# Kernel optimization log

Hardware: AMD Instinct MI355X
Metric: run time of the kernel (lower is better)

Reference implementation:

```python
import jax, jax.numpy as jnp
import numpy as np

B, L = 512, 260          # batch, raw input length
N_EMB, E_DIM = 8192, 128 * 65
NC = 16                   # num_classes


def setup_inputs() -> dict:
    key = jax.random.key(0)
    ks = jax.random.split(key, 12)
    rn = lambda k, shp, s: jax.random.normal(k, shp, jnp.float32) * s
    return {
        "x": rn(ks[0], (B, L), 1.0),
        # VQ codebook, init uniform(-1/K, 1/K) as in reference VQ-VAE
        "codebook": jax.random.uniform(ks[1], (N_EMB, E_DIM), jnp.float32, -1.0 / N_EMB, 1.0 / N_EMB),
        # encoder: Conv1d(1,64,k4,s2,p1) -> ReLU -> Conv1d(64,128,k4,s2,p1)
        "conv1_w": rn(ks[2], (64, 1, 4), 0.3), "conv1_b": jnp.zeros((64,), jnp.float32),
        "conv2_w": rn(ks[3], (128, 64, 4), 0.06), "conv2_b": jnp.zeros((128,), jnp.float32),
        # decoder: ConvT1d(128,64,k4,s2,p1) -> ReLU -> ConvT1d(64,1,k4,s2,p1); torch weight layout (in,out,k)
        "dec1_w": rn(ks[4], (128, 64, 4), 0.04), "dec1_b": jnp.zeros((64,), jnp.float32),
        "dec2_w": rn(ks[5], (64, 1, 4), 0.06), "dec2_b": jnp.zeros((1,), jnp.float32),
        # multitask head: Linear(4160, NC); torch layout (out,in)
        "mt_w": rn(ks[6], (NC, 4160), 0.015), "mt_b": jnp.zeros((NC,), jnp.float32),
        # adversary head: Linear(4160,256)->ReLU->Linear(256,128)->ReLU->Linear(128,NC)
        "adv_w1": rn(ks[7], (256, 4160), 0.015), "adv_b1": jnp.zeros((256,), jnp.float32),
        "adv_w2": rn(ks[8], (128, 256), 0.06), "adv_b2": jnp.zeros((128,), jnp.float32),
        "adv_w3": rn(ks[9], (NC, 128), 0.09), "adv_b3": jnp.zeros((NC,), jnp.float32),
        "beta": 0.25,
    }


def _conv1d(x, w, b, stride):
    # x: [B,C,L], w: [O,I,K] (torch Conv1d layout), padding=1
    y = jax.lax.conv_general_dilated(x, w, (stride,), [(1, 1)],
                                     dimension_numbers=("NCH", "OIH", "NCH"))
    return y + b[None, :, None]


def _convT1d(x, w, b, stride, k=4, p=1):
    # torch ConvTranspose1d(in,out,k,stride=s,padding=p); w: [I,O,K]
    # == dilated conv with lhs_dilation=s, padding=k-1-p, spatially-flipped, IO-swapped kernel
    wt = jnp.flip(w, -1).transpose(1, 0, 2)  # [O,I,K]
    pad = k - 1 - p
    y = jax.lax.conv_general_dilated(x, wt, (1,), [(pad, pad)], lhs_dilation=(stride,),
                                     dimension_numbers=("NCH", "OIH", "NCH"))
    return y + b[None, :, None]


def _forward(x, codebook, conv1_w, conv1_b, conv2_w, conv2_b,
             dec1_w, dec1_b, dec2_w, dec2_b, mt_w, mt_b,
             adv_w1, adv_b1, adv_w2, adv_b2, adv_w3, adv_b3, beta):
    sg = jax.lax.stop_gradient
    xb = x[:, None, :]                                      # x.unsqueeze_(1) -> [B,1,260]
    h = jax.nn.relu(_conv1d(xb, conv1_w, conv1_b, 2))       # [B,64,130]
    z_e = _conv1d(h, conv2_w, conv2_b, 2)                   # [B,128,65]
    b = z_e.shape[0]

    # ---- VectorQuantizer: cdist^2 / argmin / gather / commitment loss ----
    z = z_e.reshape(b, -1)                                  # [B,8320]
    d = (jnp.sum(z * z, axis=1, keepdims=True)
         + jnp.sum(codebook * codebook, axis=1)[None, :]
         - 2.0 * (z @ codebook.T))                          # [B,N_EMB]
    idx = jnp.argmin(d, axis=1)                             # [B]
    zq_raw = codebook[idx].reshape(z_e.shape)               # gather -> [B,128,65]
    emb_loss = (jnp.mean((sg(zq_raw) - z_e) ** 2)
                + beta * jnp.mean((zq_raw - sg(z_e)) ** 2))
    z_q = z_e + sg(zq_raw - z_e)                            # straight-through
    counts = jnp.zeros((codebook.shape[0],), z.dtype).at[idx].add(1.0)
    e_mean = counts / b
    perplexity = jnp.exp(-jnp.sum(e_mean * jnp.log(e_mean + 1e-10)))

    # ---- heads operate on z_e halves ----
    mt = z_e[:, :64, :].reshape(b, -1) @ mt_w.T + mt_b      # [B,NC]
    a = jax.nn.relu(z_e[:, 64:, :].reshape(b, -1) @ adv_w1.T + adv_b1)
    a = jax.nn.relu(a @ adv_w2.T + adv_b2)
    adv = a @ adv_w3.T + adv_b3                             # [B,NC]

    # ---- decoder on quantized codes ----
    hd = jax.nn.relu(_convT1d(z_q, dec1_w, dec1_b, 2))      # [B,64,130]
    x_hat = _convT1d(hd, dec2_w, dec2_b, 2)                 # [B,1,260]
    return emb_loss, x_hat, mt, adv, perplexity


def reference(x, codebook, conv1_w, conv1_b, conv2_w, conv2_b,
              dec1_w, dec1_b, dec2_w, dec2_b, mt_w, mt_b,
              adv_w1, adv_b1, adv_w2, adv_b2, adv_w3, adv_b3, beta):
    return _forward(x, codebook, conv1_w, conv1_b, conv2_w, conv2_b,
                    dec1_w, dec1_b, dec2_w, dec2_b, mt_w, mt_b,
                    adv_w1, adv_b1, adv_w2, adv_b2, adv_w3, adv_b3, beta)
```

## Files before the change

kernel.cpp:

```cpp
#include <hip/hip_runtime.h>
#include <stdint.h>

typedef __attribute__((ext_vector_type(8))) short s8v;
typedef __attribute__((ext_vector_type(4))) float f4v;

#define OUT_XHAT 1
#define OUT_MT   133121
#define OUT_ADV  141313
#define OUT_PERP 149505

#define WS_COUNTS   0
#define WS_EMB      8192
#define WS_A1       8256
#define WS_CN       139328
#define WS_ZN2      147520
#define WS_ZL1      148032
#define WS_CBL1     148544
#define WS_ZERO_N   156736
#define WS_ZE       156736
#define WS_SC0      4416576
#define WS_SC1      8610880
#define WS_HD       8676416
#define WS_W2T      12936256
#define WS_WE       12969024
#define WS_WO       12985408
#define WS_W2TA     13001792
#define WS_IDX      13034560
#define WS_ZPK      13035136
#define WS_CBT      15165056

__device__ __forceinline__ short f2bf(float f) {
  uint32_t u = __float_as_uint(f);
  u = (u + 0x7FFFu + ((u >> 16) & 1u)) >> 16;
  return (short)u;
}

__device__ __forceinline__ void gl_lds16(const void* g, void* l) {
  __builtin_amdgcn_global_load_lds(
      (const __attribute__((address_space(1))) void*)g,
      (__attribute__((address_space(3))) void*)l, 16, 0, 0);
}

__global__ void k_initprep(float* __restrict__ W, const float* __restrict__ c2w,
                           const float* __restrict__ d1w,
                           const float* __restrict__ aw2) {
  int id = blockIdx.x * 256 + threadIdx.x;
  if (id < WS_ZERO_N) W[id] = 0.f;
  float* w2t = W + WS_W2T;
  float* We = W + WS_WE;
  float* Wo = W + WS_WO;
  float* w2ta = W + WS_W2TA;
  if (id < 32768) {
    int c = id & 127, ik = id >> 7;
    int i = ik >> 2, k = ik & 3;
    w2t[id] = c2w[(c * 64 + i) * 4 + k];
    int kk = id >> 7;
    w2ta[id] = aw2[(id & 127) * 256 + kk];
  }
  if (id < 16384) {
    int o = id & 63, is = id >> 6;
    int i = is >> 1, s = is & 1;
    We[id] = d1w[(i * 64 + o) * 4 + (3 - 2 * s)];
    Wo[id] = d1w[(i * 64 + o) * 4 + (2 - 2 * s)];
  }
}

__device__ __forceinline__ void packmat_body(
    const float* __restrict__ src, short* __restrict__ dst,
    float* __restrict__ nrm2, float* __restrict__ l1, int R, int nb, int bid,
    int tid, short* tile, float* rsq, float* rl1) {
  int n0 = (bid % nb) * 64;
  int k0 = (bid / nb) * 64;
  int nr = tid >> 2, qc = tid & 3;
  const float* sp = src + (size_t)(n0 + nr) * 8320 + k0 + qc * 16;
  float v[16];
  *(float4*)&v[0] = *(const float4*)(sp);
  *(float4*)&v[4] = *(const float4*)(sp + 4);
  *(float4*)&v[8] = *(const float4*)(sp + 8);
  *(float4*)&v[12] = *(const float4*)(sp + 12);
  float sq = 0.f, sl = 0.f;
#pragma unroll
  for (int i = 0; i < 16; ++i) {
    sq = fmaf(v[i], v[i], sq);
    sl += fabsf(v[i]);
  }
  union { short s[8]; int4 q; } u0, u1;
#pragma unroll
  for (int j = 0; j < 8; ++j) {
    u0.s[j] = f2bf(v[j]);
    u1.s[j] = f2bf(v[8 + j]);
  }
  *(int4*)&tile[((qc * 2 + 0) * 64 + nr) * 8] = u0.q;
  *(int4*)&tile[((qc * 2 + 1) * 64 + nr) * 8] = u1.q;
  rsq[tid] = sq;
  rl1[tid] = sl;
  __syncthreads();
  if (tid < 64) {
    float s = rsq[tid * 4] + rsq[tid * 4 + 1] + rsq[tid * 4 + 2] + rsq[tid * 4 + 3];
    float t = rl1[tid * 4] + rl1[tid * 4 + 1] + rl1[tid * 4 + 2] + rl1[tid * 4 + 3];
    atomicAdd(&nrm2[n0 + tid], s);
    atomicAdd(&l1[n0 + tid], t);
  }
  int kc = tid >> 5, nn = (tid & 31) * 2;
  size_t ob = ((size_t)(k0 / 8 + kc) * R + n0 + nn) * 8;
  *(int4*)&dst[ob] = *(int4*)&tile[(kc * 64 + nn) * 8];
  *(int4*)&dst[ob + 8] = *(int4*)&tile[(kc * 64 + nn + 1) * 8];
}

__global__ __launch_bounds__(256) void k_megaA(
    const float* __restrict__ x, const float* __restrict__ c1w,
    const float* __restrict__ c1b, const float* __restrict__ w2t,
    const float* __restrict__ c2b, float* __restrict__ zebuf,
    const float* __restrict__ cb, short* __restrict__ cbt,
    float* __restrict__ cn, float* __restrict__ cbl1) {
  __shared__ __align__(16) char smem[28032];
  int bid = blockIdx.x, tid = threadIdx.x;
  if (bid < 520) {
    float* At = (float*)smem;
    float* Bt = At + 2048;
    float* xs = Bt + 4096;
    float* w1s = xs + 520;
    float* b1s = w1s + 256;
    int row0 = bid * 64;
    int tm = (tid & 15) * 4;
    int tn = (tid >> 4) * 8;
    int sr = tid & 63;
    int sj0 = (tid >> 6) * 8;
    int rowm = row0 + sr;
    int gb = rowm / 65;
    int gt = rowm - gb * 65;
    int gb0 = row0 / 65;
    int xrow = gb - gb0;
    int tpos = 2 * gt - 1;
    int bkr = tid >> 3;
    int bnc = (tid & 7) * 16;
    for (int u = tid; u < 520; u += 256) {
      int rr = gb0 + (u >= 260 ? 1 : 0);
      if (rr > 511) rr = 511;
      xs[u] = x[rr * 260 + (u >= 260 ? u - 260 : u)];
    }
    if (tid < 256) w1s[tid] = c1w[tid];
    if (tid < 64) b1s[tid] = c1b[tid];
    __syncthreads();
    float acc[4][8];
#pragma unroll
    for (int i = 0; i < 4; ++i)
#pragma unroll
      for (int j = 0; j < 8; ++j) acc[i][j] = 0.f;
    for (int k0i = 0; k0i < 256; k0i += 32) {
      float av[8];
#pragma unroll
      for (int u = 0; u < 8; ++u) {
        int jj = k0i + sj0 + u;
        int cc = jj >> 2;
        int kk = jj & 3;
        int p = tpos + kk;
        float hv = 0.f;
        if (p >= 0 && p < 130) {
          float a = b1s[cc];
          int base = 2 * p - 1;
#pragma unroll
          for (int k = 0; k < 4; ++k) {
            int xp = base + k;
            float xv = (xp >= 0 && xp < 260) ? xs[xrow * 260 + xp] : 0.f;
            a = fmaf(xv, w1s[cc * 4 + k], a);
          }
          hv = fmaxf(a, 0.f);
        }
        av[u] = hv;
      }
      float bvv[16];
#pragma unroll
      for (int u = 0; u < 16; ++u) bvv[u] = w2t[(k0i + bkr) * 128 + bnc + u];
      __syncthreads();
#pragma unroll
      for (int u = 0; u < 8; ++u) At[(sj0 + u) * 64 + sr] = av[u];
#pragma unroll
      for (int u = 0; u < 16; ++u) Bt[bkr * 128 + bnc + u] = bvv[u];
      __syncthreads();
#pragma unroll
      for (int kk = 0; kk < 32; ++kk) {
        float a0 = At[kk * 64 + tm + 0];
        float a1 = At[kk * 64 + tm + 1];
        float a2 = At[kk * 64 + tm + 2];
        float a3 = At[kk * 64 + tm + 3];
#pragma unroll
        for (int j = 0; j < 8; ++j) {
          float bv = Bt[kk * 128 + tn + j];
          acc[0][j] = fmaf(a0, bv, acc[0][j]);
          acc[1][j] = fmaf(a1, bv, acc[1][j]);
          acc[2][j] = fmaf(a2, bv, acc[2][j]);
          acc[3][j] = fmaf(a3, bv, acc[3][j]);
        }
      }
    }
#pragma unroll
    for (int i = 0; i < 4; ++i) {
      int rr = row0 + tm + i;
      int b = rr / 65, t = rr - b * 65;
#pragma unroll
      for (int j = 0; j < 8; ++j) {
        int n = tn + j;
        zebuf[(size_t)b * 8320 + (size_t)n * 65 + t] = acc[i][j] + c2b[n];
      }
    }
  } else {
    short* tile = (short*)smem;
    float* rsq = (float*)(smem + 8192);
    float* rl1 = rsq + 256;
    packmat_body(cb, cbt, cn, cbl1, 8192, 128, bid - 520, tid, tile, rsq, rl1);
  }
}

__global__ __launch_bounds__(256) void k_megaB(
    const float* __restrict__ z_e, const float* __restrict__ mtw,
    const float* __restrict__ mtb, const float* __restrict__ aw1,
    short* __restrict__ zpk, float* __restrict__ zn2, float* __restrict__ zl1,
    float* __restrict__ a1, float* __restrict__ out) {
  __shared__ __align__(16) char smem[16384];
  int bid = blockIdx.x, tid = threadIdx.x;
  if (bid < 320) {
    float* At = (float*)smem;
    float* Bt = At + 2048;
    int ksp = bid % 10;
    int nt = (bid / 10) & 3;
    int mt = bid / 40;
    int m0 = mt * 64, n0 = nt * 64, kb = ksp * 416;
    int tm = (tid & 15) * 4, tn = (tid >> 4) * 4;
    int sr = tid & 63, sj = (tid >> 6) * 8;
    const float* za = z_e + (size_t)(m0 + sr) * 8320 + 4160 + kb + sj;
    const float* wb = aw1 + (size_t)(n0 + sr) * 4160 + kb + sj;
    float acc[4][4];
#pragma unroll
    for (int i = 0; i < 4; ++i)
#pragma unroll
      for (int j = 0; j < 4; ++j) acc[i][j] = 0.f;
    for (int k0 = 0; k0 < 416; k0 += 32) {
      float4 av0 = *(const float4*)(za + k0);
      float4 av1 = *(const float4*)(za + k0 + 4);
      float4 bv0 = *(const float4*)(wb + k0);
      float4 bv1 = *(const float4*)(wb + k0 + 4);
      __syncthreads();
      At[(sj + 0) * 64 + sr] = av0.x; At[(sj + 1) * 64 + sr] = av0.y;
      At[(sj + 2) * 64 + sr] = av0.z; At[(sj + 3) * 64 + sr] = av0.w;
      At[(sj + 4) * 64 + sr] = av1.x; At[(sj + 5) * 64 + sr] = av1.y;
      At[(sj + 6) * 64 + sr] = av1.z; At[(sj + 7) * 64 + sr] = av1.w;
      Bt[(sj + 0) * 64 + sr] = bv0.x; Bt[(sj + 1) * 64 + sr] = bv0.y;
      Bt[(sj + 2) * 64 + sr] = bv0.z; Bt[(sj + 3) * 64 + sr] = bv0.w;
      Bt[(sj + 4) * 64 + sr] = bv1.x; Bt[(sj + 5) * 64 + sr] = bv1.y;
      Bt[(sj + 6) * 64 + sr] = bv1.z; Bt[(sj + 7) * 64 + sr] = bv1.w;
      __syncthreads();
#pragma unroll
      for (int kk = 0; kk < 32; ++kk) {
        float4 aa = *(const float4*)&At[kk * 64 + tm];
        float4 bb = *(const float4*)&Bt[kk * 64 + tn];
        acc[0][0] = fmaf(aa.x, bb.x, acc[0][0]); acc[0][1] = fmaf(aa.x, bb.y, acc[0][1]);
        acc[0][2] = fmaf(aa.x, bb.z, acc[0][2]); acc[0][3] = fmaf(aa.x, bb.w, acc[0][3]);
        acc[1][0] = fmaf(aa.y, bb.x, acc[1][0]); acc[1][1] = fmaf(aa.y, bb.y, acc[1][1]);
        acc[1][2] = fmaf(aa.y, bb.z, acc[1][2]); acc[1][3] = fmaf(aa.y, bb.w, acc[1][3]);
        acc[2][0] = fmaf(aa.z, bb.x, acc[2][0]); acc[2][1] = fmaf(aa.z, bb.y, acc[2][1]);
        acc[2][2] = fmaf(aa.z, bb.z, acc[2][2]); acc[2][3] = fmaf(aa.z, bb.w, acc[2][3]);
        acc[3][0] = fmaf(aa.w, bb.x, acc[3][0]); acc[3][1] = fmaf(aa.w, bb.y, acc[3][1]);
        acc[3][2] = fmaf(aa.w, bb.z, acc[3][2]); acc[3][3] = fmaf(aa.w, bb.w, acc[3][3]);
      }
    }
#pragma unroll
    for (int i = 0; i < 4; ++i)
#pragma unroll
      for (int j = 0; j < 4; ++j)
        atomicAdd(&a1[(size_t)(m0 + tm + i) * 256 + n0 + tn + j], acc[i][j]);
  } else if (bid < 832) {
    float* red = (float*)smem;
    int b = bid - 320;
    int wave = tid >> 6, lane = tid & 63;
    const float* zr = z_e + (size_t)b * 8320;
    float acc[16];
#pragma unroll
    for (int n = 0; n < 16; ++n) acc[n] = 0.f;
    for (int k4 = tid; k4 < 1040; k4 += 256) {
      float4 zv = *(const float4*)&zr[k4 * 4];
#pragma unroll
      for (int n = 0; n < 16; ++n) {
        float4 wv = *(const float4*)&mtw[n * 4160 + k4 * 4];
        float a = acc[n];
        a = fmaf(zv.x, wv.x, a);
        a = fmaf(zv.y, wv.y, a);
        a = fmaf(zv.z, wv.z, a);
        a = fmaf(zv.w, wv.w, a);
        acc[n] = a;
      }
    }
#pragma unroll
    for (int n = 0; n < 16; ++n) {
      float v = acc[n];
      for (int off = 32; off > 0; off >>= 1) v += __shfl_down(v, off);
      if (lane == 0) red[n * 4 + wave] = v;
    }
    __syncthreads();
    if (tid < 16) {
      float s = red[tid * 4] + red[tid * 4 + 1] + red[tid * 4 + 2] + red[tid * 4 + 3];
      out[OUT_MT + b * 16 + tid] = s + mtb[tid];
    }
  } else {
    short* tile = (short*)smem;
    float* rsq = (float*)(smem + 8192);
    float* rl1 = rsq + 256;
    packmat_body(z_e, zpk, zn2, zl1, 512, 8, bid - 832, tid, tile, rsq, rl1);
  }
}

__global__ __launch_bounds__(256) void k_scores(const short* __restrict__ cbt,
                                                const short* __restrict__ zpk,
                                                const float* __restrict__ cn,
                                                float* __restrict__ sc0,
                                                float* __restrict__ sc1) {
  __shared__ short As[8 * 128 * 8];
  __shared__ short Bs[8 * 128 * 8];
  int bid = blockIdx.x;
  int kh = bid & 1, nt = (bid >> 1) & 63, mt = bid >> 7;
  int tid = threadIdx.x;
  int wave = tid >> 6, lane = tid & 63;
  int q = lane >> 4, r16 = lane & 15;
  int m0 = mt * 128, n0 = nt * 128;
  int cb8 = kh * 520;
  int rb = (wave >> 1) * 64, cw = (wave & 1) * 64;

  f4v acc[4][4];
#pragma unroll
  for (int i = 0; i < 4; ++i)
#pragma unroll
    for (int j = 0; j < 4; ++j)
#pragma unroll
      for (int r = 0; r < 4; ++r) acc[i][j][r] = 0.f;

  for (int ks = 0; ks < 65; ++ks) {
    int c0 = cb8 + ks * 8;
    __syncthreads();
#pragma unroll
    for (int i = 0; i < 4; ++i) {
      int kc = wave * 2 + (i & 1);
      int h = (i >> 1) * 64;
      size_t gk = (size_t)(c0 + kc);
      gl_lds16(zpk + (gk * 512 + m0 + h + lane) * 8, &As[(kc * 128 + h) * 8]);
      gl_lds16(cbt + (gk * 8192 + n0 + h + lane) * 8, &Bs[(kc * 128 + h) * 8]);
    }
    __syncthreads();
    s8v af[2][4], bfr[2][4];
#pragma unroll
    for (int g = 0; g < 2; ++g) {
      int kq = (g * 4 + q) * 128;
#pragma unroll
      for (int i = 0; i < 4; ++i) {
        af[g][i] = *(const s8v*)&As[(kq + rb + i * 16 + r16) * 8];
        bfr[g][i] = *(const s8v*)&Bs[(kq + cw + i * 16 + r16) * 8];
      }
    }
#pragma unroll
    for (int g = 0; g < 2; ++g)
#pragma unroll
      for (int mi = 0; mi < 4; ++mi)
#pragma unroll
        for (int ni = 0; ni < 4; ++ni)
          acc[mi][ni] = __builtin_amdgcn_mfma_f32_16x16x32_bf16(
              af[g][mi], bfr[g][ni], acc[mi][ni], 0, 0, 0);
  }

  float* sc = kh ? sc1 : sc0;
#pragma unroll
  for (int mi = 0; mi < 4; ++mi) {
#pragma unroll
    for (int ni = 0; ni < 4; ++ni) {
      int col = n0 + cw + ni * 16 + r16;
      float cnv = kh ? 0.f : cn[col];
#pragma unroll
      for (int r = 0; r < 4; ++r) {
        int row = m0 + rb + mi * 16 + q * 4 + r;
        sc[(size_t)row * 8192 + col] = -2.f * acc[mi][ni][r] + cnv;
      }
    }
  }
}

__global__ __launch_bounds__(256) void k_argming(
    const float* __restrict__ s0, const float* __restrict__ s1,
    const float* __restrict__ z_e, const float* __restrict__ cb,
    const float* __restrict__ zn2, const float* __restrict__ cn,
    int* __restrict__ idx, float* __restrict__ counts,
    float* __restrict__ emb_acc) {
  __shared__ float srow[8192];
  __shared__ float red[256];
  __shared__ int cand[128];
  __shared__ float cval[128];
  __shared__ int ccnt;
  __shared__ int bsel;
  int b = blockIdx.x, tid = threadIdx.x;
  const float* r0 = s0 + (size_t)b * 8192;
  const float* r1 = s1 + (size_t)b * 8192;
  float mn = 1e30f;
  for (int j4 = tid; j4 < 2048; j4 += 256) {
    float4 a = *(const float4*)&r0[j4 * 4];
    float4 c = *(const float4*)&r1[j4 * 4];
    float4 v;
    v.x = a.x + c.x; v.y = a.y + c.y; v.z = a.z + c.z; v.w = a.w + c.w;
    *(float4*)&srow[j4 * 4] = v;
    mn = fminf(mn, fminf(fminf(v.x, v.y), fminf(v.z, v.w)));
  }
  red[tid] = mn;
  __syncthreads();
  for (int st = 128; st > 0; st >>= 1) {
    if (tid < st) red[tid] = fminf(red[tid], red[tid + st]);
    __syncthreads();
  }
  float minv = red[0];
  float margin = sqrtf(zn2[b]) * (1.0f / 131072.0f) + 1e-4f;
  if (tid == 0) ccnt = 0;
  __syncthreads();
  float thr = minv + margin;
  for (int j = tid; j < 8192; j += 256) {
    if (srow[j] <= thr) {
      int p = atomicAdd(&ccnt, 1);
      if (p < 128) cand[p] = j;
    }
  }
  __syncthreads();
  int nc = min(ccnt, 128);
  int wave = tid >> 6, lane = tid & 63;
  const float* zr = z_e + (size_t)b * 8320;
  float zn = zn2[b];
  for (int ci = wave; ci < nc; ci += 4) {
    int j = cand[ci];
    const float* cr = cb + (size_t)j * 8320;
    float dp = 0.f;
    for (int k4 = lane; k4 < 2080; k4 += 64) {
      float4 zv = *(const float4*)&zr[k4 * 4];
      float4 cv = *(const float4*)&cr[k4 * 4];
      dp = fmaf(zv.x, cv.x, dp);
      dp = fmaf(zv.y, cv.y, dp);
      dp = fmaf(zv.z, cv.z, dp);
      dp = fmaf(zv.w, cv.w, dp);
    }
    for (int off = 32; off > 0; off >>= 1) dp += __shfl_down(dp, off);
    if (lane == 0)
      cval[ci] = __fsub_rn(__fadd_rn(zn, cn[j]), __fmul_rn(2.f, dp));
  }
  __syncthreads();
  if (tid == 0) {
    float bv = 1e30f;
    int bj = 0x7fffffff;
    for (int ci = 0; ci < nc; ++ci) {
      float v = cval[ci];
      int j = cand[ci];
      if (v < bv || (v == bv && j < bj)) { bv = v; bj = j; }
    }
    idx[b] = bj;
    atomicAdd(&counts[bj], 1.0f);
    bsel = bj;
  }
  __syncthreads();
  int bj = bsel;
  const float* cr2 = cb + (size_t)bj * 8320;
  float part = 0.f;
  for (int k4 = tid; k4 < 2080; k4 += 256) {
    float4 cv = *(const float4*)&cr2[k4 * 4];
    float4 zv = *(const float4*)&zr[k4 * 4];
    float d0 = cv.x - zv.x, d1 = cv.y - zv.y;
    float d2 = cv.z - zv.z, d3 = cv.w - zv.w;
    part += d0 * d0 + d1 * d1 + d2 * d2 + d3 * d3;
  }
  red[tid] = part;
  __syncthreads();
  for (int st = 128; st > 0; st >>= 1) {
    if (tid < st) red[tid] += red[tid + st];
    __syncthreads();
  }
  if (tid == 0) atomicAdd(emb_acc, red[0]);
}

__global__ __launch_bounds__(256) void k_dec1both(
    const float* __restrict__ cb, const int* __restrict__ idxb,
    const float* __restrict__ We, const float* __restrict__ Wo,
    const float* __restrict__ bias, float* __restrict__ hd) {
  __shared__ float At[32 * 64];
  __shared__ float Bt[32 * 64];
  int bid = blockIdx.x, tid = threadIdx.x;
  int par = (bid >= 520) ? 1 : 0;
  int bl = bid - par * 520;
  const float* wt = par ? Wo : We;
  int toff = par - 1;
  int row0 = bl * 64;
  int tm = (tid & 15) * 4, tn = (tid >> 4) * 4;
  int sr = tid & 63, sj0 = (tid >> 6) * 8;
  int rowm = row0 + sr;
  int gb = rowm / 65, gt = rowm - gb * 65;
  const float* sbase = cb + (size_t)idxb[gb] * 8320;
  int tpos = gt + toff;
  int bkr = tid >> 3, bnc = (tid & 7) * 8;
  float acc[4][4];
#pragma unroll
  for (int i = 0; i < 4; ++i)
#pragma unroll
    for (int j = 0; j < 4; ++j) acc[i][j] = 0.f;
  for (int k0 = 0; k0 < 256; k0 += 32) {
    float av[8];
#pragma unroll
    for (int u = 0; u < 8; ++u) {
      int jj = k0 + sj0 + u;
      int cc = jj >> 1;
      int kk = jj & 1;
      int p = tpos + kk;
      av[u] = (p >= 0 && p < 65) ? sbase[cc * 65 + p] : 0.f;
    }
    float bvv[8];
#pragma unroll
    for (int u = 0; u < 8; ++u) bvv[u] = wt[(k0 + bkr) * 64 + bnc + u];
    __syncthreads();
#pragma unroll
    for (int u = 0; u < 8; ++u) At[(sj0 + u) * 64 + sr] = av[u];
#pragma unroll
    for (int u = 0; u < 8; ++u) Bt[bkr * 64 + bnc + u] = bvv[u];
    __syncthreads();
#pragma unroll
    for (int kk = 0; kk < 32; ++kk) {
      float a0 = At[kk * 64 + tm + 0];
      float a1 = At[kk * 64 + tm + 1];
      float a2 = At[kk * 64 + tm + 2];
      float a3 = At[kk * 64 + tm + 3];
#pragma unroll
      for (int j = 0; j < 4; ++j) {
        float bv = Bt[kk * 64 + tn + j];
        acc[0][j] = fmaf(a0, bv, acc[0][j]);
        acc[1][j] = fmaf(a1, bv, acc[1][j]);
        acc[2][j] = fmaf(a2, bv, acc[2][j]);
        acc[3][j] = fmaf(a3, bv, acc[3][j]);
      }
    }
  }
#pragma unroll
  for (int i = 0; i < 4; ++i) {
    int rr = row0 + tm + i;
    int b = rr / 65, t = rr - b * 65;
#pragma unroll
    for (int j = 0; j < 4; ++j) {
      int n = tn + j;
      float v = fmaxf(acc[i][j] + bias[n], 0.f);
      hd[(size_t)b * 8320 + (size_t)n * 130 + t * 2 + par] = v;
    }
  }
}

__global__ void k_megaC(const float* __restrict__ hd, const float* __restrict__ d2w,
                        const float* __restrict__ d2b,
                        const float* __restrict__ a1raw, const float* __restrict__ b1,
                        const float* __restrict__ w2ta, const float* __restrict__ b2,
                        const float* __restrict__ w3, const float* __restrict__ b3,
                        const float* __restrict__ counts,
                        const float* __restrict__ emb_acc,
                        const float* __restrict__ beta_p, float* __restrict__ out) {
  __shared__ float sbuf[384];
  int bid = blockIdx.x, tid = threadIdx.x;
  if (bid < 520) {
    int id = bid * 256 + tid;
    if (id >= 512 * 260) return;
    int b = id / 260, t = id % 260;
    int u = t >> 1;
    const float* hb = hd + (size_t)b * 8320;
    float acc = d2b[0];
    if (t & 1) {
      bool ok = (u + 1 < 130);
      for (int i = 0; i < 64; ++i) {
        acc = fmaf(hb[i * 130 + u], d2w[i * 4 + 2], acc);
        if (ok) acc = fmaf(hb[i * 130 + u + 1], d2w[i * 4 + 0], acc);
      }
    } else {
      bool ok = (u >= 1);
      for (int i = 0; i < 64; ++i) {
        if (ok) acc = fmaf(hb[i * 130 + u - 1], d2w[i * 4 + 3], acc);
        acc = fmaf(hb[i * 130 + u], d2w[i * 4 + 1], acc);
      }
    }
    out[OUT_XHAT + id] = acc;
  } else if (bid < 1032) {
    float* s1 = sbuf;
    float* s2 = sbuf + 256;
    int b = bid - 520;
    s1[tid] = fmaxf(a1raw[(size_t)b * 256 + tid] + b1[tid], 0.f);
    __syncthreads();
    if (tid < 128) {
      float acc = b2[tid];
      for (int k = 0; k < 256; ++k) acc = fmaf(s1[k], w2ta[k * 128 + tid], acc);
      s2[tid] = fmaxf(acc, 0.f);
    }
    __syncthreads();
    if (tid < 16) {
      float acc = b3[tid];
      for (int k = 0; k < 128; ++k) acc = fmaf(s2[k], w3[tid * 128 + k], acc);
      out[OUT_ADV + b * 16 + tid] = acc;
    }
  } else {
    float* red = sbuf;
    float part = 0.f;
    for (int j = tid; j < 8192; j += 256) {
      float e = counts[j] * (1.0f / 512.0f);
      part += e * logf(e + 1e-10f);
    }
    red[tid] = part;
    __syncthreads();
    for (int st = 128; st > 0; st >>= 1) {
      if (tid < st) red[tid] += red[tid + st];
      __syncthreads();
    }
    if (tid == 0) {
      out[OUT_PERP] = expf(-red[0]);
      out[0] = (1.f + beta_p[0]) * emb_acc[0] * (1.0f / 4259840.0f);
    }
  }
}

extern "C" void kernel_launch(void* const* d_in, const int* in_sizes, int n_in,
                              void* d_out, int out_size, void* d_ws, size_t ws_size,
                              hipStream_t stream) {
  (void)in_sizes; (void)n_in; (void)out_size; (void)ws_size;
  const float* x   = (const float*)d_in[0];
  const float* cb  = (const float*)d_in[1];
  const float* c1w = (const float*)d_in[2];
  const float* c1b = (const float*)d_in[3];
  const float* c2w = (const float*)d_in[4];
  const float* c2b = (const float*)d_in[5];
  const float* d1w = (const float*)d_in[6];
  const float* d1b = (const float*)d_in[7];
  const float* d2w = (const float*)d_in[8];
  const float* d2b = (const float*)d_in[9];
  const float* mtw = (const float*)d_in[10];
  const float* mtb = (const float*)d_in[11];
  const float* aw1 = (const float*)d_in[12];
  const float* ab1 = (const float*)d_in[13];
  const float* aw2 = (const float*)d_in[14];
  const float* ab2 = (const float*)d_in[15];
  const float* aw3 = (const float*)d_in[16];
  const float* ab3 = (const float*)d_in[17];
  const float* beta = (const float*)d_in[18];
  (void)aw2;
  float* out = (float*)d_out;
  float* W = (float*)d_ws;

  float* counts = W + WS_COUNTS;
  float* embac  = W + WS_EMB;
  float* a1buf  = W + WS_A1;
  float* cnbuf  = W + WS_CN;
  float* zn2    = W + WS_ZN2;
  float* zl1    = W + WS_ZL1;
  float* cbl1   = W + WS_CBL1;
  float* zebuf  = W + WS_ZE;
  float* sc0    = W + WS_SC0;
  float* sc1    = W + WS_SC1;
  float* hdbuf  = W + WS_HD;
  float* w2t    = W + WS_W2T;
  float* We     = W + WS_WE;
  float* Wo     = W + WS_WO;
  float* w2ta   = W + WS_W2TA;
  int*   idxb   = (int*)(W + WS_IDX);
  short* zpk    = (short*)(W + WS_ZPK);
  short* cbt    = (short*)(W + WS_CBT);

  k_initprep<<<613, 256, 0, stream>>>(W, c2w, d1w, aw2);
  k_megaA<<<520 + 16640, 256, 0, stream>>>(x, c1w, c1b, w2t, c2b, zebuf,
                                           cb, cbt, cnbuf, cbl1);
  k_megaB<<<320 + 512 + 1040, 256, 0, stream>>>(zebuf, mtw, mtb, aw1,
                                                zpk, zn2, zl1, a1buf, out);
  k_scores<<<512, 256, 0, stream>>>(cbt, zpk, cnbuf, sc0, sc1);
  k_argming<<<512, 256, 0, stream>>>(sc0, sc1, zebuf, cb, zn2, cnbuf, idxb,
                                     counts, embac);
  k_dec1both<<<1040, 256, 0, stream>>>(cb, idxb, We, Wo, d1b, hdbuf);
  k_megaC<<<520 + 512 + 1, 256, 0, stream>>>(hdbuf, d2w, d2b, a1buf, ab1,
                                             w2ta, ab2, aw3, ab3, counts,
                                             embac, beta, out);
}
```

Baseline: 703.2 us.

## Replace global atomics with split-K partials and in-kernel histogram; fuse decoder parities

Replaces the atomic accumulation of the adversary first layer with per-K-split partial buffers that the head kernel sums, and swaps the global counts and embedding-loss atomics for per-batch partials plus a shared-memory histogram in the final block. It drops the unused L1-norm computations and shrinks the zeroing in the prep kernel. The decoder's even and odd output parities are now computed together in one block so the gathered codebook rows are loaded once. In exchange it uses more workspace, the last single block does more serial work, and the decoder block uses more shared memory and registers.

```diff
diff --git a/kernel.cpp b/kernel.cpp
--- a/kernel.cpp
+++ b/kernel.cpp
@@ -9,25 +9,21 @@
 #define OUT_ADV  141313
 #define OUT_PERP 149505
 
-#define WS_COUNTS   0
-#define WS_EMB      8192
-#define WS_A1       8256
-#define WS_CN       139328
-#define WS_ZN2      147520
-#define WS_ZL1      148032
-#define WS_CBL1     148544
-#define WS_ZERO_N   156736
-#define WS_ZE       156736
-#define WS_SC0      4416576
-#define WS_SC1      8610880
-#define WS_HD       8676416
-#define WS_W2T      12936256
-#define WS_WE       12969024
-#define WS_WO       12985408
-#define WS_W2TA     13001792
-#define WS_IDX      13034560
-#define WS_ZPK      13035136
-#define WS_CBT      15165056
+#define WS_EMBP     0
+#define WS_A1P      512
+#define WS_CN       1311232
+#define WS_ZN2      1319424
+#define WS_W2T      1319936
+#define WS_WE       1352704
+#define WS_WO       1369088
+#define WS_W2TA     1385472
+#define WS_IDX      1418240
+#define WS_ZE       1418752
+#define WS_SC0      5678592
+#define WS_SC1      9872896
+#define WS_HD       14067200
+#define WS_ZPK      18327040
+#define WS_CBT      20456960
 
 __device__ __forceinline__ short f2bf(float f) {
   uint32_t u = __float_as_uint(f);
@@ -45,11 +41,12 @@
                            const float* __restrict__ d1w,
                            const float* __restrict__ aw2) {
   int id = blockIdx.x * 256 + threadIdx.x;
-  if (id < WS_ZERO_N) W[id] = 0.f;
   float* w2t = W + WS_W2T;
   float* We = W + WS_WE;
   float* Wo = W + WS_WO;
   float* w2ta = W + WS_W2TA;
+  if (id < 8192) (W + WS_CN)[id] = 0.f;
+  if (id < 512) (W + WS_ZN2)[id] = 0.f;
   if (id < 32768) {
     int c = id & 127, ik = id >> 7;
     int i = ik >> 2, k = ik & 3;
@@ -67,8 +64,8 @@
 
 __device__ __forceinline__ void packmat_body(
     const float* __restrict__ src, short* __restrict__ dst,
-    float* __restrict__ nrm2, float* __restrict__ l1, int R, int nb, int bid,
-    int tid, short* tile, float* rsq, float* rl1) {
+    float* __restrict__ nrm2, int R, int nb, int bid, int tid,
+    short* tile, float* rsq) {
   int n0 = (bid % nb) * 64;
   int k0 = (bid / nb) * 64;
   int nr = tid >> 2, qc = tid & 3;
@@ -78,12 +75,9 @@
   *(float4*)&v[4] = *(const float4*)(sp + 4);
   *(float4*)&v[8] = *(const float4*)(sp + 8);
   *(float4*)&v[12] = *(const float4*)(sp + 12);
-  float sq = 0.f, sl = 0.f;
-#pragma unroll
-  for (int i = 0; i < 16; ++i) {
-    sq = fmaf(v[i], v[i], sq);
-    sl += fabsf(v[i]);
-  }
+  float sq = 0.f;
+#pragma unroll
+  for (int i = 0; i < 16; ++i) sq = fmaf(v[i], v[i], sq);
   union { short s[8]; int4 q; } u0, u1;
 #pragma unroll
   for (int j = 0; j < 8; ++j) {
@@ -93,13 +87,10 @@
   *(int4*)&tile[((qc * 2 + 0) * 64 + nr) * 8] = u0.q;
   *(int4*)&tile[((qc * 2 + 1) * 64 + nr) * 8] = u1.q;
   rsq[tid] = sq;
-  rl1[tid] = sl;
   __syncthreads();
   if (tid < 64) {
     float s = rsq[tid * 4] + rsq[tid * 4 + 1] + rsq[tid * 4 + 2] + rsq[tid * 4 + 3];
-    float t = rl1[tid * 4] + rl1[tid * 4 + 1] + rl1[tid * 4 + 2] + rl1[tid * 4 + 3];
     atomicAdd(&nrm2[n0 + tid], s);
-    atomicAdd(&l1[n0 + tid], t);
   }
   int kc = tid >> 5, nn = (tid & 31) * 2;
   size_t ob = ((size_t)(k0 / 8 + kc) * R + n0 + nn) * 8;
@@ -112,7 +103,7 @@
     const float* __restrict__ c1b, const float* __restrict__ w2t,
     const float* __restrict__ c2b, float* __restrict__ zebuf,
     const float* __restrict__ cb, short* __restrict__ cbt,
-    float* __restrict__ cn, float* __restrict__ cbl1) {
+    float* __restrict__ cn) {
   __shared__ __align__(16) char smem[28032];
   int bid = blockIdx.x, tid = threadIdx.x;
   if (bid < 520) {
@@ -207,16 +198,15 @@
   } else {
     short* tile = (short*)smem;
     float* rsq = (float*)(smem + 8192);
-    float* rl1 = rsq + 256;
-    packmat_body(cb, cbt, cn, cbl1, 8192, 128, bid - 520, tid, tile, rsq, rl1);
+    packmat_body(cb, cbt, cn, 8192, 128, bid - 520, tid, tile, rsq);
   }
 }
 
 __global__ __launch_bounds__(256) void k_megaB(
     const float* __restrict__ z_e, const float* __restrict__ mtw,
     const float* __restrict__ mtb, const float* __restrict__ aw1,
-    short* __restrict__ zpk, float* __restrict__ zn2, float* __restrict__ zl1,
-    float* __restrict__ a1, float* __restrict__ out) {
+    short* __restrict__ zpk, float* __restrict__ zn2,
+    float* __restrict__ a1p, float* __restrict__ out) {
   __shared__ __align__(16) char smem[16384];
   int bid = blockIdx.x, tid = threadIdx.x;
   if (bid < 320) {
@@ -268,7 +258,7 @@
     for (int i = 0; i < 4; ++i)
 #pragma unroll
       for (int j = 0; j < 4; ++j)
-        atomicAdd(&a1[(size_t)(m0 + tm + i) * 256 + n0 + tn + j], acc[i][j]);
+        a1p[((size_t)ksp * 512 + m0 + tm + i) * 256 + n0 + tn + j] = acc[i][j];
   } else if (bid < 832) {
     float* red = (float*)smem;
     int b = bid - 320;
@@ -304,8 +294,7 @@
   } else {
     short* tile = (short*)smem;
     float* rsq = (float*)(smem + 8192);
-    float* rl1 = rsq + 256;
-    packmat_body(z_e, zpk, zn2, zl1, 512, 8, bid - 832, tid, tile, rsq, rl1);
+    packmat_body(z_e, zpk, zn2, 512, 8, bid - 832, tid, tile, rsq);
   }
 }
 
@@ -385,8 +374,7 @@
     const float* __restrict__ s0, const float* __restrict__ s1,
     const float* __restrict__ z_e, const float* __restrict__ cb,
     const float* __restrict__ zn2, const float* __restrict__ cn,
-    int* __restrict__ idx, float* __restrict__ counts,
-    float* __restrict__ emb_acc) {
+    int* __restrict__ idx, float* __restrict__ embp) {
   __shared__ float srow[8192];
   __shared__ float red[256];
   __shared__ int cand[128];
@@ -453,7 +441,6 @@
       if (v < bv || (v == bv && j < bj)) { bv = v; bj = j; }
     }
     idx[b] = bj;
-    atomicAdd(&counts[bj], 1.0f);
     bsel = bj;
   }
   __syncthreads();
@@ -473,65 +460,75 @@
     if (tid < st) red[tid] += red[tid + st];
     __syncthreads();
   }
-  if (tid == 0) atomicAdd(emb_acc, red[0]);
+  if (tid == 0) embp[b] = red[0];
 }
 
 __global__ __launch_bounds__(256) void k_dec1both(
     const float* __restrict__ cb, const int* __restrict__ idxb,
     const float* __restrict__ We, const float* __restrict__ Wo,
     const float* __restrict__ bias, float* __restrict__ hd) {
-  __shared__ float At[32 * 64];
-  __shared__ float Bt[32 * 64];
+  __shared__ float Ae[32 * 64];
+  __shared__ float Ao[32 * 64];
+  __shared__ float Be[32 * 64];
+  __shared__ float Bo[32 * 64];
   int bid = blockIdx.x, tid = threadIdx.x;
-  int par = (bid >= 520) ? 1 : 0;
-  int bl = bid - par * 520;
-  const float* wt = par ? Wo : We;
-  int toff = par - 1;
-  int row0 = bl * 64;
+  int row0 = bid * 64;
   int tm = (tid & 15) * 4, tn = (tid >> 4) * 4;
   int sr = tid & 63, sj0 = (tid >> 6) * 8;
   int rowm = row0 + sr;
   int gb = rowm / 65, gt = rowm - gb * 65;
   const float* sbase = cb + (size_t)idxb[gb] * 8320;
-  int tpos = gt + toff;
   int bkr = tid >> 3, bnc = (tid & 7) * 8;
-  float acc[4][4];
+  float ae[4][4], ao[4][4];
 #pragma unroll
   for (int i = 0; i < 4; ++i)
 #pragma unroll
-    for (int j = 0; j < 4; ++j) acc[i][j] = 0.f;
+    for (int j = 0; j < 4; ++j) { ae[i][j] = 0.f; ao[i][j] = 0.f; }
   for (int k0 = 0; k0 < 256; k0 += 32) {
-    float av[8];
+    float ave[8], avo[8];
+#pragma unroll
+    for (int u = 0; u < 8; u += 2) {
+      int cc = (k0 + sj0 + u) >> 1;
+      const float* cp = sbase + cc * 65;
+      float vm = (gt >= 1) ? cp[gt - 1] : 0.f;
+      float v0 = cp[gt];
+      float vp = (gt + 1 < 65) ? cp[gt + 1] : 0.f;
+      ave[u] = vm; ave[u + 1] = v0;
+      avo[u] = v0; avo[u + 1] = vp;
+    }
+    float bve[8], bvo[8];
 #pragma unroll
     for (int u = 0; u < 8; ++u) {
-      int jj = k0 + sj0 + u;
-      int cc = jj >> 1;
-      int kk = jj & 1;
-      int p = tpos + kk;
-      av[u] = (p >= 0 && p < 65) ? sbase[cc * 65 + p] : 0.f;
-    }
-    float bvv[8];
-#pragma unroll
-    for (int u = 0; u < 8; ++u) bvv[u] = wt[(k0 + bkr) * 64 + bnc + u];
-    __syncthreads();
-#pragma unroll
-    for (int u = 0; u < 8; ++u) At[(sj0 + u) * 64 + sr] = av[u];
-#pragma unroll
-    for (int u = 0; u < 8; ++u) Bt[bkr * 64 + bnc + u] = bvv[u];
+      bve[u] = We[(k0 + bkr) * 64 + bnc + u];
+      bvo[u] = Wo[(k0 + bkr) * 64 + bnc + u];
+    }
+    __syncthreads();
+#pragma unroll
+    for (int u = 0; u < 8; ++u) {
+      Ae[(sj0 + u) * 64 + sr] = ave[u];
+      Ao[(sj0 + u) * 64 + sr] = avo[u];
+      Be[bkr * 64 + bnc + u] = bve[u];
+      Bo[bkr * 64 + bnc + u] = bvo[u];
+    }
     __syncthreads();
 #pragma unroll
     for (int kk = 0; kk < 32; ++kk) {
-      float a0 = At[kk * 64 + tm + 0];
-      float a1 = At[kk * 64 + tm + 1];
-      float a2 = At[kk * 64 + tm + 2];
-      float a3 = At[kk * 64 + tm + 3];
+      float e0 = Ae[kk * 64 + tm + 0], e1 = Ae[kk * 64 + tm + 1];
+      float e2 = Ae[kk * 64 + tm + 2], e3 = Ae[kk * 64 + tm + 3];
+      float o0 = Ao[kk * 64 + tm + 0], o1 = Ao[kk * 64 + tm + 1];
+      float o2 = Ao[kk * 64 + tm + 2], o3 = Ao[kk * 64 + tm + 3];
 #pragma unroll
       for (int j = 0; j < 4; ++j) {
-        float bv = Bt[kk * 64 + tn + j];
-        acc[0][j] = fmaf(a0, bv, acc[0][j]);
-        acc[1][j] = fmaf(a1, bv, acc[1][j]);
-        acc[2][j] = fmaf(a2, bv, acc[2][j]);
-        acc[3][j] = fmaf(a3, bv, acc[3][j]);
+        float be = Be[kk * 64 + tn + j];
+        float bo = Bo[kk * 64 + tn + j];
+        ae[0][j] = fmaf(e0, be, ae[0][j]);
+        ae[1][j] = fmaf(e1, be, ae[1][j]);
+        ae[2][j] = fmaf(e2, be, ae[2][j]);
+        ae[3][j] = fmaf(e3, be, ae[3][j]);
+        ao[0][j] = fmaf(o0, bo, ao[0][j]);
+        ao[1][j] = fmaf(o1, bo, ao[1][j]);
+        ao[2][j] = fmaf(o2, bo, ao[2][j]);
+        ao[3][j] = fmaf(o3, bo, ao[3][j]);
       }
     }
   }
@@ -542,20 +539,24 @@
 #pragma unroll
     for (int j = 0; j < 4; ++j) {
       int n = tn + j;
-      float v = fmaxf(acc[i][j] + bias[n], 0.f);
-      hd[(size_t)b * 8320 + (size_t)n * 130 + t * 2 + par] = v;
+      float bn_ = bias[n];
+      hd[(size_t)b * 8320 + (size_t)n * 130 + t * 2 + 0] =
+          fmaxf(ae[i][j] + bn_, 0.f);
+      hd[(size_t)b * 8320 + (size_t)n * 130 + t * 2 + 1] =
+          fmaxf(ao[i][j] + bn_, 0.f);
     }
   }
 }
 
 __global__ void k_megaC(const float* __restrict__ hd, const float* __restrict__ d2w,
                         const float* __restrict__ d2b,
-                        const float* __restrict__ a1raw, const float* __restrict__ b1,
+                        const float* __restrict__ a1p, const float* __restrict__ b1,
                         const float* __restrict__ w2ta, const float* __restrict__ b2,
                         const float* __restrict__ w3, const float* __restrict__ b3,
-                        const float* __restrict__ counts,
-                        const float* __restrict__ emb_acc,
+                        const int* __restrict__ idxb,
+                        const float* __restrict__ embp,
                         const float* __restrict__ beta_p, float* __restrict__ out) {
+  __shared__ int hsh[8192];
   __shared__ float sbuf[384];
   int bid = blockIdx.x, tid = threadIdx.x;
   if (bid < 520) {
@@ -583,7 +584,11 @@
     float* s1 = sbuf;
     float* s2 = sbuf + 256;
     int b = bid - 520;
-    s1[tid] = fmaxf(a1raw[(size_t)b * 256 + tid] + b1[tid], 0.f);
+    float s = b1[tid];
+    const float* ap = a1p + (size_t)b * 256 + tid;
+#pragma unroll
+    for (int p = 0; p < 10; ++p) s += ap[(size_t)p * 131072];
+    s1[tid] = fmaxf(s, 0.f);
     __syncthreads();
     if (tid < 128) {
       float acc = b2[tid];
@@ -598,20 +603,34 @@
     }
   } else {
     float* red = sbuf;
+    for (int j = tid; j < 8192; j += 256) hsh[j] = 0;
+    __syncthreads();
+    for (int i = tid; i < 512; i += 256) atomicAdd(&hsh[idxb[i]], 1);
+    __syncthreads();
     float part = 0.f;
     for (int j = tid; j < 8192; j += 256) {
-      float e = counts[j] * (1.0f / 512.0f);
+      float e = (float)hsh[j] * (1.0f / 512.0f);
       part += e * logf(e + 1e-10f);
     }
+    float ep = 0.f;
+    for (int i = tid; i < 512; i += 256) ep += embp[i];
     red[tid] = part;
     __syncthreads();
     for (int st = 128; st > 0; st >>= 1) {
       if (tid < st) red[tid] += red[tid + st];
       __syncthreads();
     }
+    float negH = red[0];
+    __syncthreads();
+    red[tid] = ep;
+    __syncthreads();
+    for (int st = 128; st > 0; st >>= 1) {
+      if (tid < st) red[tid] += red[tid + st];
+      __syncthreads();
+    }
     if (tid == 0) {
-      out[OUT_PERP] = expf(-red[0]);
-      out[0] = (1.f + beta_p[0]) * emb_acc[0] * (1.0f / 4259840.0f);
+      out[OUT_PERP] = expf(-negH);
+      out[0] = (1.f + beta_p[0]) * red[0] * (1.0f / 4259840.0f);
     }
   }
 }
@@ -639,39 +658,35 @@
   const float* aw3 = (const float*)d_in[16];
   const float* ab3 = (const float*)d_in[17];
   const float* beta = (const float*)d_in[18];
-  (void)aw2;
   float* out = (float*)d_out;
   float* W = (float*)d_ws;
 
-  float* counts = W + WS_COUNTS;
-  float* embac  = W + WS_EMB;
-  float* a1buf  = W + WS_A1;
+  float* embp   = W + WS_EMBP;
+  float* a1p    = W + WS_A1P;
   float* cnbuf  = W + WS_CN;
   float* zn2    = W + WS_ZN2;
-  float* zl1    = W + WS_ZL1;
-  float* cbl1   = W + WS_CBL1;
-  float* zebuf  = W + WS_ZE;
-  float* sc0    = W + WS_SC0;
-  float* sc1    = W + WS_SC1;
-  float* hdbuf  = W + WS_HD;
   float* w2t    = W + WS_W2T;
   float* We     = W + WS_WE;
   float* Wo     = W + WS_WO;
   float* w2ta   = W + WS_W2TA;
   int*   idxb   = (int*)(W + WS_IDX);
+  float* zebuf  = W + WS_ZE;
+  float* sc0    = W + WS_SC0;
+  float* sc1    = W + WS_SC1;
+  float* hdbuf  = W + WS_HD;
   short* zpk    = (short*)(W + WS_ZPK);
   short* cbt    = (short*)(W + WS_CBT);
 
-  k_initprep<<<613, 256, 0, stream>>>(W, c2w, d1w, aw2);
+  k_initprep<<<128, 256, 0, stream>>>(W, c2w, d1w, aw2);
   k_megaA<<<520 + 16640, 256, 0, stream>>>(x, c1w, c1b, w2t, c2b, zebuf,
-                                           cb, cbt, cnbuf, cbl1);
+                                           cb, cbt, cnbuf);
   k_megaB<<<320 + 512 + 1040, 256, 0, stream>>>(zebuf, mtw, mtb, aw1,
-                                                zpk, zn2, zl1, a1buf, out);
+                                                zpk, zn2, a1p, out);
   k_scores<<<512, 256, 0, stream>>>(cbt, zpk, cnbuf, sc0, sc1);
   k_argming<<<512, 256, 0, stream>>>(sc0, sc1, zebuf, cb, zn2, cnbuf, idxb,
-                                     counts, embac);
-  k_dec1both<<<1040, 256, 0, stream>>>(cb, idxb, We, Wo, d1b, hdbuf);
-  k_megaC<<<520 + 512 + 1, 256, 0, stream>>>(hdbuf, d2w, d2b, a1buf, ab1,
-                                             w2ta, ab2, aw3, ab3, counts,
-                                             embac, beta, out);
-}
+                                     embp);
+  k_dec1both<<<520, 256, 0, stream>>>(cb, idxb, We, Wo, d1b, hdbuf);
+  k_megaC<<<520 + 512 + 1, 256, 0, stream>>>(hdbuf, d2w, d2b, a1p, ab1,
+                                             w2ta, ab2, aw3, ab3, idxb,
+                                             embp, beta, out);
+}
```

Result: no change. 693.9 us (-1.3%).
